# Performance work log

Measured on AMD Instinct MI355X. Metric: run time of the kernel, lower is better.

Reference implementation:

```python
import jax, jax.numpy as jnp
import numpy as np

N_NODES = 100000
D_FEAT = 128
UNITS = 128
N_EDGES = 600000


def setup_inputs() -> dict:
    key = jax.random.key(0)
    k1, k2, k3, k4, k5 = jax.random.split(key, 5)
    X = jax.random.normal(k1, (N_NODES, D_FEAT), dtype=jnp.float32)
    ref_a = jax.random.randint(k2, (N_EDGES,), 0, N_NODES, dtype=jnp.int32)
    ref_b = jax.random.randint(k3, (N_EDGES,), 0, N_NODES, dtype=jnp.int32)
    # Glorot-ish scaled dense weights
    W_hidden = jax.random.normal(k4, (D_FEAT, UNITS), dtype=jnp.float32) * (1.0 / np.sqrt(D_FEAT))
    W_out = jax.random.normal(k5, (UNITS, UNITS), dtype=jnp.float32) * (1.0 / np.sqrt(UNITS))
    b_hidden = jnp.zeros((UNITS,), dtype=jnp.float32)
    b_out = jnp.zeros((UNITS,), dtype=jnp.float32)
    return dict(X=X, ref_a=ref_a, ref_b=ref_b, W_hidden=W_hidden,
                b_hidden=b_hidden, W_out=W_out, b_out=b_out)


def wl1_convolution(X, ref_a, ref_b):
    # WL1 neighborhood aggregation over undirected edges (ref_a, ref_b):
    # each node keeps its own features plus the sum of its neighbors'.
    n = X.shape[0]
    agg_a = jax.ops.segment_sum(X[ref_b], ref_a, num_segments=n)  # [N, D]
    agg_b = jax.ops.segment_sum(X[ref_a], ref_b, num_segments=n)  # [N, D]
    return X + agg_a + agg_b


def reference(X, ref_a, ref_b, W_hidden, b_hidden, W_out, b_out):
    X_agg = wl1_convolution(X, ref_a, ref_b)                 # [N, D]
    X_hid = jax.nn.relu(X_agg @ W_hidden + b_hidden)          # [N, U] (inner_activation=relu)
    X_out = X_hid @ W_out + b_out                             # [N, U] (activation=linear)
    return X_out
```

## Files before the change

kernel.cpp:

```cpp
#include <hip/hip_runtime.h>

#define CAP 64
#define BCAP 4096
#define RADIX_UNITS 4096

typedef short bf16x8 __attribute__((ext_vector_type(8)));
typedef float f32x4 __attribute__((ext_vector_type(4)));
typedef unsigned short u16;
typedef unsigned int u32;

__device__ __forceinline__ u16 f32_to_bf16(float f) {
  u32 b = __float_as_uint(f);
  b += 0x7fffu + ((b >> 16) & 1u);
  return (u16)(b >> 16);
}

__global__ __launch_bounds__(256) void front_kernel(
    const float* __restrict__ X, u16* __restrict__ Xb, int n8,
    const int* __restrict__ ra, const int* __restrict__ rb,
    int* __restrict__ gOff, int2* __restrict__ binned, int nedges, int nunits,
    int nbins, int nradix) {
  if ((int)blockIdx.x >= nradix) {
    int i = ((int)blockIdx.x - nradix) * 256 + threadIdx.x;
    if (i >= n8) return;
    float4 a = ((const float4*)X)[2 * i];
    float4 b = ((const float4*)X)[2 * i + 1];
    int4 o;
    o.x = (int)((u32)f32_to_bf16(a.x) | ((u32)f32_to_bf16(a.y) << 16));
    o.y = (int)((u32)f32_to_bf16(a.z) | ((u32)f32_to_bf16(a.w) << 16));
    o.z = (int)((u32)f32_to_bf16(b.x) | ((u32)f32_to_bf16(b.y) << 16));
    o.w = (int)((u32)f32_to_bf16(b.z) | ((u32)f32_to_bf16(b.w) << 16));
    ((int4*)Xb)[i] = o;
    return;
  }
  __shared__ int lh[512];
  const int tid = threadIdx.x;
  for (int b = tid; b < nbins; b += 256) lh[b] = 0;
  __syncthreads();
  const int u0 = (int)blockIdx.x * RADIX_UNITS;

  for (int k = 0; k < RADIX_UNITS / 256; ++k) {
    int u = u0 + k * 256 + tid;
    if (u < nunits) {
      long long apk = ((const long long*)ra)[u];
      long long bpk = ((const long long*)rb)[u];
      int a0 = (int)apk, a1 = (int)(apk >> 32);
      int b0 = (int)bpk, b1 = (int)(bpk >> 32);
      bool has1 = (2 * u + 1) < nedges;
      atomicAdd(&lh[a0 >> 8], 1);
      atomicAdd(&lh[b0 >> 8], 1);
      if (has1) {
        atomicAdd(&lh[a1 >> 8], 1);
        atomicAdd(&lh[b1 >> 8], 1);
      }
    }
  }
  __syncthreads();
  for (int b = tid; b < nbins; b += 256) {
    int c = lh[b];
    lh[b] = (c > 0) ? atomicAdd(&gOff[b], c) : 0;
  }
  __syncthreads();
  for (int k = 0; k < RADIX_UNITS / 256; ++k) {
    int u = u0 + k * 256 + tid;
    if (u < nunits) {
      long long apk = ((const long long*)ra)[u];
      long long bpk = ((const long long*)rb)[u];
      int a0 = (int)apk, a1 = (int)(apk >> 32);
      int b0 = (int)bpk, b1 = (int)(bpk >> 32);
      bool has1 = (2 * u + 1) < nedges;
      int d[4], s[4];
      d[0] = a0; s[0] = b0;
      d[1] = b0; s[1] = a0;
      d[2] = has1 ? a1 : -1; s[2] = b1;
      d[3] = has1 ? b1 : -1; s[3] = a1;
#pragma unroll
      for (int i = 0; i < 4; ++i) {
        if (d[i] >= 0) {
          int b = d[i] >> 8;
          int slot = atomicAdd(&lh[b], 1);
          if (slot < BCAP) binned[(size_t)b * BCAP + slot] = make_int2(d[i], s[i]);
        }
      }
    }
  }
}

__global__ __launch_bounds__(256) void bin_build_kernel(
    const int2* __restrict__ binned, const int* __restrict__ gOff,
    int* __restrict__ cnt, int* __restrict__ adj, int nnodes) {
  __shared__ int lc[256];
  const int bin = blockIdx.x;
  lc[threadIdx.x] = 0;
  __syncthreads();
  int count = gOff[bin];
  if (count > BCAP) count = BCAP;
  const int2* src = binned + (size_t)bin * BCAP;
  for (int i = threadIdx.x; i < count; i += 256) {
    int2 e = src[i];
    int p = atomicAdd(&lc[e.x & 255], 1);
    if (p < CAP) adj[(size_t)e.x * CAP + p] = e.y;
  }
  __syncthreads();
  int node = bin * 256 + threadIdx.x;
  if (node < nnodes) cnt[node] = lc[threadIdx.x];
}

__global__ void gather_agg_kernel(const u16* __restrict__ Xb,
                                  const int* __restrict__ cnt,
                                  int* __restrict__ adj, int nnodes) {
  int gid = blockIdx.x * blockDim.x + threadIdx.x;
  int wid = gid >> 6;
  int l = gid & 63;
  int q = l >> 4;
  int ql = l & 15;
  int node = wid * 4 + q;
  if (node >= nnodes) return;
  const uint4* Xv = (const uint4*)Xb;
  const int* lst = adj + (size_t)node * CAP;
  int n = cnt[node];
  if (n > CAP) n = CAP;
  int idx0 = lst[ql];
  int idx1 = (n > 16) ? lst[ql + 16] : 0;
  int idx2 = (n > 32) ? lst[ql + 32] : 0;
  int idx3 = (n > 48) ? lst[ql + 48] : 0;
  uint4 ps = Xv[(size_t)node * 16 + ql];
  float acc[8];
  acc[0] = __uint_as_float(ps.x << 16);
  acc[1] = __uint_as_float(ps.x & 0xffff0000u);
  acc[2] = __uint_as_float(ps.y << 16);
  acc[3] = __uint_as_float(ps.y & 0xffff0000u);
  acc[4] = __uint_as_float(ps.z << 16);
  acc[5] = __uint_as_float(ps.z & 0xffff0000u);
  acc[6] = __uint_as_float(ps.w << 16);
  acc[7] = __uint_as_float(ps.w & 0xffff0000u);
  const int base = q << 4;
  for (int k = 0; k < n; k += 16) {
    uint4 pv[16];
#pragma unroll
    for (int t = 0; t < 16; ++t) {
      int pos = k + t;
      int sel = (pos < 16) ? idx0 : (pos < 32) ? idx1 : (pos < 48) ? idx2 : idx3;
      int nb = __shfl(sel, base + (pos & 15));
      pv[t] = (pos < n) ? Xv[(size_t)nb * 16 + ql] : make_uint4(0u, 0u, 0u, 0u);
    }
#pragma unroll
    for (int t = 0; t < 16; ++t) {
      acc[0] += __uint_as_float(pv[t].x << 16);
      acc[1] += __uint_as_float(pv[t].x & 0xffff0000u);
      acc[2] += __uint_as_float(pv[t].y << 16);
      acc[3] += __uint_as_float(pv[t].y & 0xffff0000u);
      acc[4] += __uint_as_float(pv[t].z << 16);
      acc[5] += __uint_as_float(pv[t].z & 0xffff0000u);
      acc[6] += __uint_as_float(pv[t].w << 16);
      acc[7] += __uint_as_float(pv[t].w & 0xffff0000u);
    }
  }
  uint4 o;
  o.x = (u32)f32_to_bf16(acc[0]) | ((u32)f32_to_bf16(acc[1]) << 16);
  o.y = (u32)f32_to_bf16(acc[2]) | ((u32)f32_to_bf16(acc[3]) << 16);
  o.z = (u32)f32_to_bf16(acc[4]) | ((u32)f32_to_bf16(acc[5]) << 16);
  o.w = (u32)f32_to_bf16(acc[6]) | ((u32)f32_to_bf16(acc[7]) << 16);
  ((uint4*)adj)[(size_t)node * 16 + ql] = o;
}

__global__ void convert_w_kernel(const float* __restrict__ Wh,
                                 const float* __restrict__ Wo,
                                 u16* __restrict__ WhT,
                                 u16* __restrict__ WoT) {
  int idx = blockIdx.x * 256 + threadIdx.x;
  const float* src = (idx < 16384) ? Wh : Wo;
  u16* dst = (idx < 16384) ? WhT : WoT;
  int i = idx & 16383;
  int k = i >> 7, n = i & 127;
  dst[n * 128 + k] = f32_to_bf16(src[k * 128 + n]);
}

__global__ __launch_bounds__(256) void mlp_mfma_kernel(
    const u16* __restrict__ Xagg,
    const u16* __restrict__ WhT,
    const u16* __restrict__ WoT,
    const float* __restrict__ bh,
    const float* __restrict__ bo,
    float* __restrict__ out, int nnodes) {
  __shared__ u16 smem[2 * 128 * 128];
  u16* sA = smem;
  u16* sW = smem + 16384;

  const int tid = threadIdx.x;
  const int w = tid >> 6;
  const int l = tid & 63;
  const int l15 = l & 15;
  const int l4 = l >> 4;
  const int r0 = blockIdx.x * 128;

#pragma unroll
  for (int t = 0; t < 8; ++t) {
    int id = tid + t * 256;
    int r = id >> 4, u = id & 15;
    int gr = r0 + r;
    if (gr >= nnodes) gr = nnodes - 1;
    *(int4*)&sA[r * 128 + ((u ^ (r & 15)) * 8)] =
        *(const int4*)&Xagg[(size_t)gr * 128 + u * 8];
    *(int4*)&sW[r * 128 + ((u ^ (r & 15)) * 8)] =
        *(const int4*)&WhT[r * 128 + u * 8];
  }

  float bhv[8], bov[8];
#pragma unroll
  for (int j = 0; j < 8; ++j) {
    bhv[j] = bh[j * 16 + l15];
    bov[j] = bo[j * 16 + l15];
  }
  __syncthreads();

  const int m0 = w * 32 + l15;
  const int m1 = w * 32 + 16 + l15;

  f32x4 acc[2][8];
#pragma unroll
  for (int i = 0; i < 2; ++i)
#pragma unroll
    for (int j = 0; j < 8; ++j) acc[i][j] = (f32x4){0.f, 0.f, 0.f, 0.f};

#pragma unroll
  for (int c = 0; c < 4; ++c) {
    int pu = ((c * 4 + l4) ^ l15) * 8;
    bf16x8 a0 = *(bf16x8*)&sA[m0 * 128 + pu];
    bf16x8 a1 = *(bf16x8*)&sA[m1 * 128 + pu];
#pragma unroll
    for (int j = 0; j < 8; ++j) {
      bf16x8 bfr = *(bf16x8*)&sW[(j * 16 + l15) * 128 + pu];
      acc[0][j] = __builtin_amdgcn_mfma_f32_16x16x32_bf16(a0, bfr, acc[0][j], 0, 0, 0);
      acc[1][j] = __builtin_amdgcn_mfma_f32_16x16x32_bf16(a1, bfr, acc[1][j], 0, 0, 0);
    }
  }

  __syncthreads();

#pragma unroll
  for (int t = 0; t < 8; ++t) {
    int id = tid + t * 256;
    int r = id >> 4, u = id & 15;
    *(int4*)&sW[r * 128 + ((u ^ (r & 15)) * 8)] =
        *(const int4*)&WoT[r * 128 + u * 8];
  }

#pragma unroll
  for (int i = 0; i < 2; ++i)
#pragma unroll
    for (int j = 0; j < 8; ++j)
#pragma unroll
      for (int r = 0; r < 4; ++r) {
        int m = w * 32 + i * 16 + l4 * 4 + r;
        float v = fmaxf(acc[i][j][r] + bhv[j], 0.f);
        int k = j * 16 + l15;
        sA[m * 128 + (((k >> 3) ^ (m & 15)) * 8) + (k & 7)] = f32_to_bf16(v);
      }
  __syncthreads();

#pragma unroll
  for (int i = 0; i < 2; ++i)
#pragma unroll
    for (int j = 0; j < 8; ++j) acc[i][j] = (f32x4){0.f, 0.f, 0.f, 0.f};

#pragma unroll
  for (int c = 0; c < 4; ++c) {
    int pu = ((c * 4 + l4) ^ l15) * 8;
    bf16x8 a0 = *(bf16x8*)&sA[m0 * 128 + pu];
    bf16x8 a1 = *(bf16x8*)&sA[m1 * 128 + pu];
#pragma unroll
    for (int j = 0; j < 8; ++j) {
      bf16x8 bfr = *(bf16x8*)&sW[(j * 16 + l15) * 128 + pu];
      acc[0][j] = __builtin_amdgcn_mfma_f32_16x16x32_bf16(a0, bfr, acc[0][j], 0, 0, 0);
      acc[1][j] = __builtin_amdgcn_mfma_f32_16x16x32_bf16(a1, bfr, acc[1][j], 0, 0, 0);
    }
  }

  __syncthreads();

  float* sOut = (float*)smem;
#pragma unroll
  for (int i = 0; i < 2; ++i)
#pragma unroll
    for (int j = 0; j < 8; ++j)
#pragma unroll
      for (int r = 0; r < 4; ++r) {
        int m = w * 32 + i * 16 + l4 * 4 + r;
        sOut[m * 128 + j * 16 + l15] = acc[i][j][r] + bov[j];
      }
  __syncthreads();
#pragma unroll
  for (int t = 0; t < 16; ++t) {
    int id = tid + t * 256;
    int r = id >> 5, u4 = id & 31;
    int gr = r0 + r;
    if (gr < nnodes)
      ((float4*)out)[(size_t)gr * 32 + u4] = ((const float4*)sOut)[id];
  }
}

extern "C" void kernel_launch(void* const* d_in, const int* in_sizes, int n_in,
                              void* d_out, int out_size, void* d_ws,
                              size_t ws_size, hipStream_t stream) {
  const float* X = (const float*)d_in[0];
  const int* ra = (const int*)d_in[1];
  const int* rb = (const int*)d_in[2];
  const float* Wh = (const float*)d_in[3];
  const float* bh = (const float*)d_in[4];
  const float* Wo = (const float*)d_in[5];
  const float* bo = (const float*)d_in[6];
  float* out = (float*)d_out;

  int nnodes = in_sizes[0] / 128;
  int nedges = in_sizes[1];
  int nunits = (nedges + 1) / 2;
  int nbins = (nnodes + 255) >> 8;
  int nradix = (nunits + RADIX_UNITS - 1) / RADIX_UNITS;

  int* cnt = (int*)d_ws;
  int* adj = cnt + nnodes;
  u16* WhT = (u16*)d_ws;
  u16* WoT = WhT + 16384;
  u16* Xb = (u16*)d_out;
  int2* binned = (int2*)((char*)d_out + (size_t)nnodes * 256);
  int* gOff = (int*)((char*)binned + (size_t)nbins * BCAP * sizeof(int2));

  int n8 = nnodes * 16;
  int nconv = (n8 + 255) / 256;
  hipMemsetAsync(gOff, 0, (size_t)nbins * 4, stream);
  front_kernel<<<nradix + nconv, 256, 0, stream>>>(
      X, Xb, n8, ra, rb, gOff, binned, nedges, nunits, nbins, nradix);
  bin_build_kernel<<<nbins, 256, 0, stream>>>(binned, gOff, cnt, adj, nnodes);
  int nwaves4 = (nnodes + 3) / 4;
  gather_agg_kernel<<<(nwaves4 * 64 + 255) / 256, 256, 0, stream>>>(
      Xb, cnt, adj, nnodes);
  convert_w_kernel<<<128, 256, 0, stream>>>(Wh, Wo, WhT, WoT);
  mlp_mfma_kernel<<<(nnodes + 127) / 128, 256, 0, stream>>>(
      (const u16*)adj, WhT, WoT, bh, bo, out, nnodes);
}
```

Measured before the change: 214.7 us.

## Slice bf16 features by XCC and gather per-slice with work-stealing queues

Stores the bf16 copy of X as 8 column slices of 32 bytes each. The gather kernel reads the hardware XCC id so that each XCC works mainly on its own slice, with an atomic chunk queue per slice for load balancing. The intent is to keep each slice's random neighbour reads inside one XCC's L2 instead of spreading whole rows across all dies. Adjacency lists shrink to 32 entries, and extra neighbours go to a global overflow list that is scanned linearly. The aggregated output uses a new interleaved layout split across the workspace and the output buffer, and the MLP is launched twice so it does not overwrite the part of the output buffer that still holds aggregated data.

```diff
diff --git a/kernel.cpp b/kernel.cpp
--- a/kernel.cpp
+++ b/kernel.cpp
@@ -1,11 +1,14 @@
 #include <hip/hip_runtime.h>
 
-#define CAP 64
-#define BCAP 4096
+#define LCAP 32
+#define BCAP 3584
 #define RADIX_UNITS 4096
+#define OVFCAP 2048
 
 typedef short bf16x8 __attribute__((ext_vector_type(8)));
 typedef float f32x4 __attribute__((ext_vector_type(4)));
+typedef int i32x4 __attribute__((ext_vector_type(4)));
+typedef unsigned int u32x4 __attribute__((ext_vector_type(4)));
 typedef unsigned short u16;
 typedef unsigned int u32;
 
@@ -15,8 +18,15 @@
   return (u16)(b >> 16);
 }
 
+__device__ __forceinline__ int comp8(const i32x4& A, const i32x4& B, int c) {
+  switch (c) {
+    case 0: return A[0]; case 1: return A[1]; case 2: return A[2]; case 3: return A[3];
+    case 4: return B[0]; case 5: return B[1]; case 6: return B[2]; default: return B[3];
+  }
+}
+
 __global__ __launch_bounds__(256) void front_kernel(
-    const float* __restrict__ X, u16* __restrict__ Xb, int n8,
+    const float* __restrict__ X, char* __restrict__ xb, size_t xbsl, int n8,
     const int* __restrict__ ra, const int* __restrict__ rb,
     int* __restrict__ gOff, int2* __restrict__ binned, int nedges, int nunits,
     int nbins, int nradix) {
@@ -30,7 +40,8 @@
     o.y = (int)((u32)f32_to_bf16(a.z) | ((u32)f32_to_bf16(a.w) << 16));
     o.z = (int)((u32)f32_to_bf16(b.x) | ((u32)f32_to_bf16(b.y) << 16));
     o.w = (int)((u32)f32_to_bf16(b.z) | ((u32)f32_to_bf16(b.w) << 16));
-    ((int4*)Xb)[i] = o;
+    int v = i >> 4, u = i & 15;
+    *(int4*)(xb + (size_t)(u >> 1) * xbsl + (size_t)v * 32 + (u & 1) * 16) = o;
     return;
   }
   __shared__ int lh[512];
@@ -42,8 +53,8 @@
   for (int k = 0; k < RADIX_UNITS / 256; ++k) {
     int u = u0 + k * 256 + tid;
     if (u < nunits) {
-      long long apk = ((const long long*)ra)[u];
-      long long bpk = ((const long long*)rb)[u];
+      long long apk = __builtin_nontemporal_load((const long long*)ra + u);
+      long long bpk = __builtin_nontemporal_load((const long long*)rb + u);
       int a0 = (int)apk, a1 = (int)(apk >> 32);
       int b0 = (int)bpk, b1 = (int)(bpk >> 32);
       bool has1 = (2 * u + 1) < nedges;
@@ -64,8 +75,8 @@
   for (int k = 0; k < RADIX_UNITS / 256; ++k) {
     int u = u0 + k * 256 + tid;
     if (u < nunits) {
-      long long apk = ((const long long*)ra)[u];
-      long long bpk = ((const long long*)rb)[u];
+      long long apk = __builtin_nontemporal_load((const long long*)ra + u);
+      long long bpk = __builtin_nontemporal_load((const long long*)rb + u);
       int a0 = (int)apk, a1 = (int)(apk >> 32);
       int b0 = (int)bpk, b1 = (int)(bpk >> 32);
       bool has1 = (2 * u + 1) < nedges;
@@ -88,7 +99,8 @@
 
 __global__ __launch_bounds__(256) void bin_build_kernel(
     const int2* __restrict__ binned, const int* __restrict__ gOff,
-    int* __restrict__ cnt, int* __restrict__ adj, int nnodes) {
+    int* __restrict__ cnt, int* __restrict__ lists, int* __restrict__ ovfCnt,
+    int2* __restrict__ ovfPairs, int nnodes) {
   __shared__ int lc[256];
   const int bin = blockIdx.x;
   lc[threadIdx.x] = 0;
@@ -99,69 +111,133 @@
   for (int i = threadIdx.x; i < count; i += 256) {
     int2 e = src[i];
     int p = atomicAdd(&lc[e.x & 255], 1);
-    if (p < CAP) adj[(size_t)e.x * CAP + p] = e.y;
+    if (p < LCAP) lists[(size_t)e.x * LCAP + p] = e.y;
+    else {
+      int o = atomicAdd(ovfCnt, 1);
+      if (o < OVFCAP) ovfPairs[o] = e;
+    }
   }
   __syncthreads();
   int node = bin * 256 + threadIdx.x;
   if (node < nnodes) cnt[node] = lc[threadIdx.x];
 }
 
-__global__ void gather_agg_kernel(const u16* __restrict__ Xb,
-                                  const int* __restrict__ cnt,
-                                  int* __restrict__ adj, int nnodes) {
-  int gid = blockIdx.x * blockDim.x + threadIdx.x;
-  int wid = gid >> 6;
-  int l = gid & 63;
-  int q = l >> 4;
-  int ql = l & 15;
-  int node = wid * 4 + q;
-  if (node >= nnodes) return;
-  const uint4* Xv = (const uint4*)Xb;
-  const int* lst = adj + (size_t)node * CAP;
-  int n = cnt[node];
-  if (n > CAP) n = CAP;
-  int idx0 = lst[ql];
-  int idx1 = (n > 16) ? lst[ql + 16] : 0;
-  int idx2 = (n > 32) ? lst[ql + 32] : 0;
-  int idx3 = (n > 48) ? lst[ql + 48] : 0;
-  uint4 ps = Xv[(size_t)node * 16 + ql];
-  float acc[8];
-  acc[0] = __uint_as_float(ps.x << 16);
-  acc[1] = __uint_as_float(ps.x & 0xffff0000u);
-  acc[2] = __uint_as_float(ps.y << 16);
-  acc[3] = __uint_as_float(ps.y & 0xffff0000u);
-  acc[4] = __uint_as_float(ps.z << 16);
-  acc[5] = __uint_as_float(ps.z & 0xffff0000u);
-  acc[6] = __uint_as_float(ps.w << 16);
-  acc[7] = __uint_as_float(ps.w & 0xffff0000u);
-  const int base = q << 4;
-  for (int k = 0; k < n; k += 16) {
-    uint4 pv[16];
-#pragma unroll
-    for (int t = 0; t < 16; ++t) {
-      int pos = k + t;
-      int sel = (pos < 16) ? idx0 : (pos < 32) ? idx1 : (pos < 48) ? idx2 : idx3;
-      int nb = __shfl(sel, base + (pos & 15));
-      pv[t] = (pos < n) ? Xv[(size_t)nb * 16 + ql] : make_uint4(0u, 0u, 0u, 0u);
-    }
-#pragma unroll
-    for (int t = 0; t < 16; ++t) {
-      acc[0] += __uint_as_float(pv[t].x << 16);
-      acc[1] += __uint_as_float(pv[t].x & 0xffff0000u);
-      acc[2] += __uint_as_float(pv[t].y << 16);
-      acc[3] += __uint_as_float(pv[t].y & 0xffff0000u);
-      acc[4] += __uint_as_float(pv[t].z << 16);
-      acc[5] += __uint_as_float(pv[t].z & 0xffff0000u);
-      acc[6] += __uint_as_float(pv[t].w << 16);
-      acc[7] += __uint_as_float(pv[t].w & 0xffff0000u);
-    }
-  }
-  uint4 o;
-  o.x = (u32)f32_to_bf16(acc[0]) | ((u32)f32_to_bf16(acc[1]) << 16);
-  o.y = (u32)f32_to_bf16(acc[2]) | ((u32)f32_to_bf16(acc[3]) << 16);
-  o.z = (u32)f32_to_bf16(acc[4]) | ((u32)f32_to_bf16(acc[5]) << 16);
-  o.w = (u32)f32_to_bf16(acc[6]) | ((u32)f32_to_bf16(acc[7]) << 16);
-  ((uint4*)adj)[(size_t)node * 16 + ql] = o;
+__global__ __launch_bounds__(256) void gather_slice_kernel(
+    const char* __restrict__ xb, size_t xbsl, const int* __restrict__ cnt,
+    const int* __restrict__ lists, const int* __restrict__ ovfCnt,
+    const int2* __restrict__ ovfPairs, int* __restrict__ q,
+    char* __restrict__ xaggD, char* __restrict__ xaggW, int nnodes,
+    int nsplit, int nchunks) {
+  const int tid = threadIdx.x;
+  const int h = tid & 1;
+  const int pl = (tid & 63) & ~1;
+  __shared__ int s_claim;
+  int x;
+  asm volatile("s_getreg_b32 %0, hwreg(HW_REG_XCC_ID)" : "=s"(x));
+  x &= 7;
+  int novf = *ovfCnt;
+  if (novf > OVFCAP) novf = OVFCAP;
+
+  for (int off = 0; off < 8; ++off) {
+    const int sl = (x + off) & 7;
+    const uint4* Xs = (const uint4*)(xb + (size_t)sl * xbsl);
+    for (;;) {
+      if (tid == 0) s_claim = atomicAdd(&q[sl], 1);
+      __syncthreads();
+      const int c = s_claim;
+      __syncthreads();
+      if (c >= nchunks) break;
+      for (int it = 0; it < 2; ++it) {
+        int v = c * 256 + it * 128 + (tid >> 1);
+        bool act = v < nnodes;
+        int n = act ? cnt[v] : 0;
+        const i32x4* lst4 = (const i32x4*)(lists + (size_t)v * LCAP);
+        i32x4 L0 = {0, 0, 0, 0}, L1 = {0, 0, 0, 0};
+        i32x4 L2 = {0, 0, 0, 0}, L3 = {0, 0, 0, 0};
+        if (act && n > 8 * h) L0 = __builtin_nontemporal_load(lst4 + 2 * h);
+        if (act && n > 8 * h + 4) L1 = __builtin_nontemporal_load(lst4 + 2 * h + 1);
+        if (act && n > 16 + 8 * h) L2 = __builtin_nontemporal_load(lst4 + 4 + 2 * h);
+        if (act && n > 20 + 8 * h) L3 = __builtin_nontemporal_load(lst4 + 5 + 2 * h);
+
+        uint4 ps = act ? Xs[(size_t)v * 2 + h] : make_uint4(0u, 0u, 0u, 0u);
+        float acc[8];
+        acc[0] = __uint_as_float(ps.x << 16);
+        acc[1] = __uint_as_float(ps.x & 0xffff0000u);
+        acc[2] = __uint_as_float(ps.y << 16);
+        acc[3] = __uint_as_float(ps.y & 0xffff0000u);
+        acc[4] = __uint_as_float(ps.z << 16);
+        acc[5] = __uint_as_float(ps.z & 0xffff0000u);
+        acc[6] = __uint_as_float(ps.w << 16);
+        acc[7] = __uint_as_float(ps.w & 0xffff0000u);
+
+#define ACCUM(P)                                          \
+  do {                                                    \
+    acc[0] += __uint_as_float((P).x << 16);               \
+    acc[1] += __uint_as_float((P).x & 0xffff0000u);       \
+    acc[2] += __uint_as_float((P).y << 16);               \
+    acc[3] += __uint_as_float((P).y & 0xffff0000u);       \
+    acc[4] += __uint_as_float((P).z << 16);               \
+    acc[5] += __uint_as_float((P).z & 0xffff0000u);       \
+    acc[6] += __uint_as_float((P).w << 16);               \
+    acc[7] += __uint_as_float((P).w & 0xffff0000u);       \
+  } while (0)
+
+        for (int pb = 0; pb < 16; pb += 8) {
+          uint4 pv[8];
+#pragma unroll
+          for (int t = 0; t < 8; ++t) {
+            int p = pb + t;
+            int val = comp8(L0, L1, p & 7);
+            int nb = __shfl(val, pl | (p >> 3));
+            bool use = act && (p < n);
+            pv[t] = use ? Xs[(size_t)nb * 2 + h] : make_uint4(0u, 0u, 0u, 0u);
+          }
+#pragma unroll
+          for (int t = 0; t < 8; ++t) ACCUM(pv[t]);
+        }
+        if (__any(n > 16)) {
+          for (int pb = 16; pb < 32; pb += 8) {
+            uint4 pv[8];
+#pragma unroll
+            for (int t = 0; t < 8; ++t) {
+              int p = pb + t;
+              int val = comp8(L2, L3, (p - 16) & 7);
+              int nb = __shfl(val, pl | ((p - 16) >> 3));
+              bool use = act && (p < n);
+              pv[t] = use ? Xs[(size_t)nb * 2 + h] : make_uint4(0u, 0u, 0u, 0u);
+            }
+#pragma unroll
+            for (int t = 0; t < 8; ++t) ACCUM(pv[t]);
+          }
+        }
+        if (__any(n > 32)) {
+          for (int j = 0; j < novf; ++j) {
+            int2 e = ovfPairs[j];
+            if (act && n > 32 && e.x == v) {
+              uint4 t4 = Xs[(size_t)e.y * 2 + h];
+              ACCUM(t4);
+            }
+          }
+        }
+#undef ACCUM
+        u32x4 o;
+        o[0] = (u32)f32_to_bf16(acc[0]) | ((u32)f32_to_bf16(acc[1]) << 16);
+        o[1] = (u32)f32_to_bf16(acc[2]) | ((u32)f32_to_bf16(acc[3]) << 16);
+        o[2] = (u32)f32_to_bf16(acc[4]) | ((u32)f32_to_bf16(acc[5]) << 16);
+        o[3] = (u32)f32_to_bf16(acc[6]) | ((u32)f32_to_bf16(acc[7]) << 16);
+        if (act) {
+          char* dst;
+          if (v < nsplit)
+            dst = xaggD + ((size_t)(v >> 2)) * 1024 + sl * 128 + (v & 3) * 32 + h * 16;
+          else {
+            int w = v - nsplit;
+            dst = xaggW + ((size_t)(w >> 2)) * 1024 + sl * 128 + (w & 3) * 32 + h * 16;
+          }
+          __builtin_nontemporal_store(o, (u32x4*)dst);
+        }
+      }
+    }
+  }
 }
 
 __global__ void convert_w_kernel(const float* __restrict__ Wh,
@@ -177,12 +253,10 @@
 }
 
 __global__ __launch_bounds__(256) void mlp_mfma_kernel(
-    const u16* __restrict__ Xagg,
-    const u16* __restrict__ WhT,
-    const u16* __restrict__ WoT,
-    const float* __restrict__ bh,
-    const float* __restrict__ bo,
-    float* __restrict__ out, int nnodes) {
+    const char* __restrict__ xaggD, const char* __restrict__ xaggW,
+    const u16* __restrict__ WhT, const u16* __restrict__ WoT,
+    const float* __restrict__ bh, const float* __restrict__ bo,
+    float* __restrict__ out, int nnodes, int nsplit, int row0) {
   __shared__ u16 smem[2 * 128 * 128];
   u16* sA = smem;
   u16* sW = smem + 16384;
@@ -192,7 +266,7 @@
   const int l = tid & 63;
   const int l15 = l & 15;
   const int l4 = l >> 4;
-  const int r0 = blockIdx.x * 128;
+  const int r0 = row0 + blockIdx.x * 128;
 
 #pragma unroll
   for (int t = 0; t < 8; ++t) {
@@ -200,8 +274,14 @@
     int r = id >> 4, u = id & 15;
     int gr = r0 + r;
     if (gr >= nnodes) gr = nnodes - 1;
-    *(int4*)&sA[r * 128 + ((u ^ (r & 15)) * 8)] =
-        *(const int4*)&Xagg[(size_t)gr * 128 + u * 8];
+    const char* xa;
+    if (gr < nsplit)
+      xa = xaggD + ((size_t)(gr >> 2)) * 1024 + (u >> 1) * 128 + (gr & 3) * 32 + (u & 1) * 16;
+    else {
+      int g = gr - nsplit;
+      xa = xaggW + ((size_t)(g >> 2)) * 1024 + (u >> 1) * 128 + (g & 3) * 32 + (u & 1) * 16;
+    }
+    *(int4*)&sA[r * 128 + ((u ^ (r & 15)) * 8)] = *(const int4*)xa;
     *(int4*)&sW[r * 128 + ((u ^ (r & 15)) * 8)] =
         *(const int4*)&WhT[r * 128 + u * 8];
   }
@@ -317,25 +397,53 @@
   int nunits = (nedges + 1) / 2;
   int nbins = (nnodes + 255) >> 8;
   int nradix = (nunits + RADIX_UNITS - 1) / RADIX_UNITS;
+  int nchunks = (nnodes + 255) / 256;
+  size_t out_bytes = (size_t)nnodes * 512;
+
+  int nsplit = (nnodes + 1) / 2;
+  nsplit = (nsplit + 3) & ~3;
+  if (nsplit > nnodes) nsplit = nnodes & ~3;
 
   int* cnt = (int*)d_ws;
-  int* adj = cnt + nnodes;
-  u16* WhT = (u16*)d_ws;
-  u16* WoT = WhT + 16384;
-  u16* Xb = (u16*)d_out;
-  int2* binned = (int2*)((char*)d_out + (size_t)nnodes * 256);
-  int* gOff = (int*)((char*)binned + (size_t)nbins * BCAP * sizeof(int2));
+  int* lists = cnt + nnodes;
+  char* xaggW = (char*)d_ws + (size_t)nnodes * 4 + (size_t)nnodes * 128;
+
+  size_t xbsl = (size_t)nnodes * 32;
+  char* xb = (char*)d_out;
+  char* binned_c = xb + 8 * xbsl;
+  size_t binned_bytes = (size_t)nbins * BCAP * 8;
+  char* CB = binned_c + ((binned_bytes + 63) & ~63ull);
+  int* q = (int*)CB;
+  int* ovfCnt = (int*)(CB + 32);
+  int* gOff = (int*)(CB + 64);
+  int2* ovfPairs = (int2*)(CB + 2048);
+  int2* binned = (int2*)binned_c;
+  char* xaggD = (char*)d_out + out_bytes - (size_t)nsplit * 256;
+
+  long long dbase = (long long)out_bytes - (long long)nsplit * 256;
+  int R1 = (int)((dbase / 512) / 128 * 128);
+  if (R1 > nnodes) R1 = ((nnodes + 127) / 128) * 128;
 
   int n8 = nnodes * 16;
   int nconv = (n8 + 255) / 256;
-  hipMemsetAsync(gOff, 0, (size_t)nbins * 4, stream);
+  (void)hipMemsetAsync(CB, 0, 2048, stream);
   front_kernel<<<nradix + nconv, 256, 0, stream>>>(
-      X, Xb, n8, ra, rb, gOff, binned, nedges, nunits, nbins, nradix);
-  bin_build_kernel<<<nbins, 256, 0, stream>>>(binned, gOff, cnt, adj, nnodes);
-  int nwaves4 = (nnodes + 3) / 4;
-  gather_agg_kernel<<<(nwaves4 * 64 + 255) / 256, 256, 0, stream>>>(
-      Xb, cnt, adj, nnodes);
-  convert_w_kernel<<<128, 256, 0, stream>>>(Wh, Wo, WhT, WoT);
-  mlp_mfma_kernel<<<(nnodes + 127) / 128, 256, 0, stream>>>(
-      (const u16*)adj, WhT, WoT, bh, bo, out, nnodes);
-}
+      X, xb, xbsl, n8, ra, rb, gOff, binned, nedges, nunits, nbins, nradix);
+  bin_build_kernel<<<nbins, 256, 0, stream>>>(binned, gOff, cnt, lists,
+                                              ovfCnt, ovfPairs, nnodes);
+  gather_slice_kernel<<<1024, 256, 0, stream>>>(
+      xb, xbsl, cnt, lists, ovfCnt, ovfPairs, q, xaggD, xaggW, nnodes, nsplit,
+      nchunks);
+  convert_w_kernel<<<128, 256, 0, stream>>>(Wh, Wo, (u16*)d_ws,
+                                            (u16*)d_ws + 16384);
+  int nb1 = R1 / 128;
+  if (nb1 > 0)
+    mlp_mfma_kernel<<<nb1, 256, 0, stream>>>(
+        xaggD, xaggW, (u16*)d_ws, (u16*)d_ws + 16384, bh, bo, out, nnodes,
+        nsplit, 0);
+  int nb2 = (nnodes - R1 + 127) / 128;
+  if (nb2 > 0)
+    mlp_mfma_kernel<<<nb2, 256, 0, stream>>>(
+        xaggD, xaggW, (u16*)d_ws, (u16*)d_ws + 16384, bh, bo, out, nnodes,
+        nsplit, R1);
+}
```

Measured after the change: 347.4 us. +61.8%, slower.
